# Optimization experiments

Measured on AMD Instinct MI355X. Metric: run time of the kernel, lower is better.

## Reference

```python
import jax, jax.numpy as jnp
import numpy as np

N_NODES = 100000
N_EDGES = 1600000
IN_CH = 128
OUT_CH = 64


def setup_inputs() -> dict:
    key = jax.random.key(0)
    k1, k2, k3, k4, k5 = jax.random.split(key, 5)
    x = jax.random.normal(k1, (N_NODES, IN_CH), dtype=jnp.float32)
    edge_index = jax.random.randint(k2, (2, N_EDGES), 0, N_NODES, dtype=jnp.int64)
    edge_weight = jax.random.uniform(k3, (N_EDGES,), dtype=jnp.float32)
    # GCNConv linear weight (glorot-ish scale) and bias
    W = jax.random.normal(k4, (IN_CH, OUT_CH), dtype=jnp.float32) / np.float32(np.sqrt(IN_CH))
    b = jax.random.normal(k5, (OUT_CH,), dtype=jnp.float32) * 0.01
    return {"x": x, "edge_index": edge_index, "edge_weight": edge_weight, "W": W, "b": b}


def reference(x, edge_index, edge_weight, W, b):
    # PyG GCNConv with add_self_loops=False, normalize=True, followed by Sigmoid.
    row = edge_index[0]  # source nodes [E]
    col = edge_index[1]  # target nodes [E]
    n = x.shape[0]

    # gcn_norm (no self loops): deg[j] = sum of edge_weight into j
    deg = jax.ops.segment_sum(edge_weight, col, num_segments=n)  # [N]
    deg_inv_sqrt = jnp.where(deg > 0, jax.lax.rsqrt(deg), jnp.float32(0))
    norm = deg_inv_sqrt[row] * edge_weight * deg_inv_sqrt[col]  # [E]

    # linear transform then gather-scale-scatter aggregation
    h = x @ W  # [N, OUT]
    msg = norm[:, None] * h[row]  # [E, OUT]
    out = jax.ops.segment_sum(msg, col, num_segments=n) + b  # [N, OUT]
    return jax.nn.sigmoid(out)
```

## Files before the change

### kernel.cpp

```cpp
#include <hip/hip_runtime.h>

#define IN_CH 128
#define OUT_CH 64
#define BN 64
#define CAP 1280
#define NPART 256

typedef __attribute__((ext_vector_type(8))) short short8;
typedef __attribute__((ext_vector_type(4))) float f32x4;

__device__ __forceinline__ unsigned short f2bf(float f) {
    unsigned u = __float_as_uint(f);
    unsigned r = (u + 0x7FFFu + ((u >> 16) & 1u)) >> 16;
    return (unsigned short)r;
}

__global__ __launch_bounds__(1024) void k_part1(const int* __restrict__ row,
                                                const int* __restrict__ col,
                                                const float* __restrict__ ew,
                                                int* __restrict__ cnt,
                                                uint2* __restrict__ sparse,
                                                int E, int per, int nbuck) {
    __shared__ int lh[1600];
    __shared__ int cur[1600];
    int tid = threadIdx.x;
    for (int i = tid; i < nbuck; i += 1024) lh[i] = 0;
    __syncthreads();
    int e0 = blockIdx.x * per;
    int e1 = min(E, e0 + per);
    for (int e = e0 + tid; e < e1; e += 1024)
        atomicAdd(&lh[col[e] >> 6], 1);
    __syncthreads();
    for (int bin = tid; bin < nbuck; bin += 1024) {
        int c = lh[bin];
        int base = c ? atomicAdd(&cnt[bin], c) : 0;
        cur[bin] = bin * CAP + base;
    }
    __syncthreads();
    int lim = nbuck * CAP;
    for (int e = e0 + tid; e < e1; e += 1024) {
        int r = row[e];
        int c = col[e];
        float w = ew[e];
        int bin = c >> 6;
        int p = atomicAdd(&cur[bin], 1);
        if (p < lim)
            sparse[p] = make_uint2((unsigned)r | ((unsigned)(c & 63) << 17),
                                   __float_as_uint(w));
    }
}

__global__ __launch_bounds__(256) void k_gemm3(const float* __restrict__ x,
                                               const float* __restrict__ W,
                                               const uint2* __restrict__ sparse,
                                               const int* __restrict__ cnt,
                                               float* __restrict__ dis,
                                               unsigned short* __restrict__ hb,
                                               int N) {
    __shared__ unsigned short Wl[64][136];
    __shared__ float degs[BN];

    int tid = threadIdx.x;
    int b = blockIdx.x;
    int row0 = b * BN;

    if (tid < BN) degs[tid] = 0.f;
    __syncthreads();

    for (int i = tid; i < 2048; i += 256) {
        int k = i >> 4;
        int n4 = (i & 15) << 2;
        float4 v = *(const float4*)(W + (size_t)k * OUT_CH + n4);
        Wl[n4 + 0][k] = f2bf(v.x);
        Wl[n4 + 1][k] = f2bf(v.y);
        Wl[n4 + 2][k] = f2bf(v.z);
        Wl[n4 + 3][k] = f2bf(v.w);
    }
    {
        int m = min(cnt[b], CAP);
        int sbase = b * CAP;
        for (int i = tid; i < m; i += 256) {
            uint2 r = sparse[sbase + i];
            atomicAdd(&degs[(r.x >> 17) & 63], __uint_as_float(r.y));
        }
    }
    __syncthreads();

    if (tid < BN) {
        float d = degs[tid];
        float dv = (d > 0.f) ? rsqrtf(d) : 0.f;
        int node = row0 + tid;
        if (node < N) dis[node] = dv;
        degs[tid] = dv;
    }

    int lane = tid & 63;
    int wv = tid >> 6;
    int r0l = 16 * wv;
    int cn = lane & 15;
    int rg = lane >> 4;

    f32x4 acc0 = {0.f, 0.f, 0.f, 0.f};
    f32x4 acc1 = {0.f, 0.f, 0.f, 0.f};
    f32x4 acc2 = {0.f, 0.f, 0.f, 0.f};
    f32x4 acc3 = {0.f, 0.f, 0.f, 0.f};

    int arow = row0 + r0l + cn;
#pragma unroll
    for (int ks = 0; ks < 4; ++ks) {
        int k0 = ks * 32 + rg * 8;
        short8 a = {};
        if (arow < N) {
            const float* xp = x + (size_t)arow * IN_CH + k0;
            float4 va = *(const float4*)(xp);
            float4 vb = *(const float4*)(xp + 4);
            a[0] = (short)f2bf(va.x); a[1] = (short)f2bf(va.y);
            a[2] = (short)f2bf(va.z); a[3] = (short)f2bf(va.w);
            a[4] = (short)f2bf(vb.x); a[5] = (short)f2bf(vb.y);
            a[6] = (short)f2bf(vb.z); a[7] = (short)f2bf(vb.w);
        }
        short8 b0 = *(const short8*)&Wl[ 0 + cn][k0];
        short8 b1 = *(const short8*)&Wl[16 + cn][k0];
        short8 b2 = *(const short8*)&Wl[32 + cn][k0];
        short8 b3 = *(const short8*)&Wl[48 + cn][k0];
        acc0 = __builtin_amdgcn_mfma_f32_16x16x32_bf16(a, b0, acc0, 0, 0, 0);
        acc1 = __builtin_amdgcn_mfma_f32_16x16x32_bf16(a, b1, acc1, 0, 0, 0);
        acc2 = __builtin_amdgcn_mfma_f32_16x16x32_bf16(a, b2, acc2, 0, 0, 0);
        acc3 = __builtin_amdgcn_mfma_f32_16x16x32_bf16(a, b3, acc3, 0, 0, 0);
    }
    __syncthreads();

#pragma unroll
    for (int r = 0; r < 4; ++r) {
        int row_l = r0l + rg * 4 + r;
        int grow = row0 + row_l;
        if (grow < N) {
            float sc = degs[row_l];
            unsigned short* hp = hb + (size_t)grow * OUT_CH + cn;
            hp[ 0] = f2bf(acc0[r] * sc);
            hp[16] = f2bf(acc1[r] * sc);
            hp[32] = f2bf(acc2[r] * sc);
            hp[48] = f2bf(acc3[r] * sc);
        }
    }
}

__global__ __launch_bounds__(256) void k_sort3(const uint2* __restrict__ sparse,
                                               const int* __restrict__ cnt,
                                               const float* __restrict__ dis,
                                               const unsigned short* __restrict__ hb,
                                               const float* __restrict__ bias,
                                               float* __restrict__ out,
                                               int N, int nbuck) {
    __shared__ uint2 recbuf[CAP];
    __shared__ uint2 recbuf2[CAP];
    __shared__ int hist[BN];
    __shared__ int cur[BN];
    __shared__ int starts[BN];

    int b = blockIdx.x;
    int tid = threadIdx.x;
    int sbase = b * CAP;
    int m = min(cnt[b], CAP);

    if (tid < BN) hist[tid] = 0;
    __syncthreads();

    for (int i = tid; i < m; i += 256) {
        uint2 r = sparse[sbase + i];
        recbuf[i] = r;
        atomicAdd(&hist[(r.x >> 17) & 63], 1);
    }
    __syncthreads();

    if (tid < 64) {
        int h = hist[tid];
        int v = h;
#pragma unroll
        for (int d = 1; d < 64; d <<= 1) {
            int t = __shfl_up(v, d, 64);
            if (tid >= d) v += t;
        }
        int excl = v - h;
        cur[tid] = excl;
        starts[tid] = excl;
    }
    __syncthreads();

    for (int i = tid; i < m; i += 256) {
        uint2 r = recbuf[i];
        int dl = (r.x >> 17) & 63;
        int p = atomicAdd(&cur[dl], 1);
        recbuf2[p] = make_uint2(r.x & 0x1FFFF, r.y);
    }
    __syncthreads();

    int hwl = tid >> 5;
    int lanep = tid & 31;
    unsigned co = 2u * (unsigned)lanep;
    for (int nl = hwl; nl < BN; nl += 8) {
        int node = b * BN + nl;
        if (node >= N) break;
        int e = starts[nl];
        int e1 = e + hist[nl];
        float accx = 0.f, accy = 0.f;
        for (; e + 3 < e1; e += 4) {
            uint2 p0 = recbuf2[e];
            uint2 p1 = recbuf2[e + 1];
            uint2 p2 = recbuf2[e + 2];
            uint2 p3 = recbuf2[e + 3];
            unsigned v0 = *(const unsigned*)(hb + (p0.x << 6) + co);
            unsigned v1 = *(const unsigned*)(hb + (p1.x << 6) + co);
            unsigned v2 = *(const unsigned*)(hb + (p2.x << 6) + co);
            unsigned v3 = *(const unsigned*)(hb + (p3.x << 6) + co);
            float w0 = __uint_as_float(p0.y), w1 = __uint_as_float(p1.y);
            float w2 = __uint_as_float(p2.y), w3 = __uint_as_float(p3.y);
            accx += w0 * __uint_as_float(v0 << 16);
            accy += w0 * __uint_as_float(v0 & 0xFFFF0000u);
            accx += w1 * __uint_as_float(v1 << 16);
            accy += w1 * __uint_as_float(v1 & 0xFFFF0000u);
            accx += w2 * __uint_as_float(v2 << 16);
            accy += w2 * __uint_as_float(v2 & 0xFFFF0000u);
            accx += w3 * __uint_as_float(v3 << 16);
            accy += w3 * __uint_as_float(v3 & 0xFFFF0000u);
        }
        for (; e < e1; ++e) {
            uint2 p = recbuf2[e];
            unsigned v = *(const unsigned*)(hb + (p.x << 6) + co);
            float w = __uint_as_float(p.y);
            accx += w * __uint_as_float(v << 16);
            accy += w * __uint_as_float(v & 0xFFFF0000u);
        }
        float dd = dis[node];
        float2 bb = *(const float2*)(bias + co);
        float2 o;
        o.x = 1.f / (1.f + __expf(-(accx * dd + bb.x)));
        o.y = 1.f / (1.f + __expf(-(accy * dd + bb.y)));
        *(float2*)(out + ((size_t)node << 6) + co) = o;
    }
}

extern "C" void kernel_launch(void* const* d_in, const int* in_sizes, int n_in,
                              void* d_out, int out_size, void* d_ws, size_t ws_size,
                              hipStream_t stream) {
    const float* x   = (const float*)d_in[0];
    const int*   ei  = (const int*)d_in[1];
    const float* ew  = (const float*)d_in[2];
    const float* W   = (const float*)d_in[3];
    const float* b   = (const float*)d_in[4];
    float* out = (float*)d_out;

    const int N = in_sizes[0] / IN_CH;
    const int E = in_sizes[1] / 2;
    const int* row = ei;
    const int* col = ei + E;

    const int nbuck = (N + BN - 1) / BN;
    const int per   = (E + NPART - 1) / NPART;

    char* p = (char*)d_ws;
    int*   cnt     = (int*)p;    p += (size_t)nbuck * 4;
    float* dis     = (float*)p;  p += (size_t)N * 4;
    uint2* sparse  = (uint2*)p;  p += (size_t)nbuck * CAP * 8;
    unsigned short* hb = (unsigned short*)p;

    hipMemsetAsync(cnt, 0, (size_t)nbuck * 4, stream);

    k_part1<<<NPART, 1024, 0, stream>>>(row, col, ew, cnt, sparse, E, per, nbuck);
    k_gemm3<<<nbuck, 256, 0, stream>>>(x, W, sparse, cnt, dis, hb, N);
    k_sort3<<<nbuck, 256, 0, stream>>>(sparse, cnt, dis, hb, b, out, N, nbuck);
}
```

Before: 199.7 us.

## Replace per-bucket counting sort with LDS float atomics in aggregation

The aggregation kernel no longer counting-sorts each bucket's edges by destination node. Instead, half-waves walk the edge records in arbitrary order and accumulate weighted bf16 features into a 64x64 float tile in shared memory with atomicAdd. A separate epilogue then applies degree scaling, bias and sigmoid with float4 stores. This removes the histogram, scan and scatter passes, at the cost of many LDS float atomics that may contend when several edges hit the same node. It also makes the summation order nondeterministic.

```diff
diff --git a/kernel.cpp b/kernel.cpp
--- a/kernel.cpp
+++ b/kernel.cpp
@@ -145,98 +145,76 @@
     }
 }
 
-__global__ __launch_bounds__(256) void k_sort3(const uint2* __restrict__ sparse,
-                                               const int* __restrict__ cnt,
-                                               const float* __restrict__ dis,
-                                               const unsigned short* __restrict__ hb,
-                                               const float* __restrict__ bias,
-                                               float* __restrict__ out,
-                                               int N, int nbuck) {
+__global__ __launch_bounds__(256) void k_agg(const uint2* __restrict__ sparse,
+                                             const int* __restrict__ cnt,
+                                             const float* __restrict__ dis,
+                                             const unsigned short* __restrict__ hb,
+                                             const float* __restrict__ bias,
+                                             float* __restrict__ out,
+                                             int N, int nbuck) {
     __shared__ uint2 recbuf[CAP];
-    __shared__ uint2 recbuf2[CAP];
-    __shared__ int hist[BN];
-    __shared__ int cur[BN];
-    __shared__ int starts[BN];
+    __shared__ float acc[BN][OUT_CH];
 
     int b = blockIdx.x;
     int tid = threadIdx.x;
     int sbase = b * CAP;
     int m = min(cnt[b], CAP);
-
-    if (tid < BN) hist[tid] = 0;
-    __syncthreads();
-
-    for (int i = tid; i < m; i += 256) {
-        uint2 r = sparse[sbase + i];
-        recbuf[i] = r;
-        atomicAdd(&hist[(r.x >> 17) & 63], 1);
-    }
-    __syncthreads();
-
-    if (tid < 64) {
-        int h = hist[tid];
-        int v = h;
-#pragma unroll
-        for (int d = 1; d < 64; d <<= 1) {
-            int t = __shfl_up(v, d, 64);
-            if (tid >= d) v += t;
-        }
-        int excl = v - h;
-        cur[tid] = excl;
-        starts[tid] = excl;
-    }
-    __syncthreads();
-
-    for (int i = tid; i < m; i += 256) {
-        uint2 r = recbuf[i];
-        int dl = (r.x >> 17) & 63;
-        int p = atomicAdd(&cur[dl], 1);
-        recbuf2[p] = make_uint2(r.x & 0x1FFFF, r.y);
-    }
-    __syncthreads();
-
-    int hwl = tid >> 5;
+    int mp = (m + 31) & ~31;
+
+    float* az = &acc[0][0];
+    for (int i = tid; i < BN * OUT_CH; i += 256) az[i] = 0.f;
+    for (int i = tid; i < mp; i += 256)
+        recbuf[i] = (i < m) ? sparse[sbase + i] : make_uint2(0u, 0u);
+    __syncthreads();
+
+    int hw = tid >> 5;
     int lanep = tid & 31;
     unsigned co = 2u * (unsigned)lanep;
-    for (int nl = hwl; nl < BN; nl += 8) {
-        int node = b * BN + nl;
-        if (node >= N) break;
-        int e = starts[nl];
-        int e1 = e + hist[nl];
-        float accx = 0.f, accy = 0.f;
-        for (; e + 3 < e1; e += 4) {
-            uint2 p0 = recbuf2[e];
-            uint2 p1 = recbuf2[e + 1];
-            uint2 p2 = recbuf2[e + 2];
-            uint2 p3 = recbuf2[e + 3];
-            unsigned v0 = *(const unsigned*)(hb + (p0.x << 6) + co);
-            unsigned v1 = *(const unsigned*)(hb + (p1.x << 6) + co);
-            unsigned v2 = *(const unsigned*)(hb + (p2.x << 6) + co);
-            unsigned v3 = *(const unsigned*)(hb + (p3.x << 6) + co);
-            float w0 = __uint_as_float(p0.y), w1 = __uint_as_float(p1.y);
-            float w2 = __uint_as_float(p2.y), w3 = __uint_as_float(p3.y);
-            accx += w0 * __uint_as_float(v0 << 16);
-            accy += w0 * __uint_as_float(v0 & 0xFFFF0000u);
-            accx += w1 * __uint_as_float(v1 << 16);
-            accy += w1 * __uint_as_float(v1 & 0xFFFF0000u);
-            accx += w2 * __uint_as_float(v2 << 16);
-            accy += w2 * __uint_as_float(v2 & 0xFFFF0000u);
-            accx += w3 * __uint_as_float(v3 << 16);
-            accy += w3 * __uint_as_float(v3 & 0xFFFF0000u);
-        }
-        for (; e < e1; ++e) {
-            uint2 p = recbuf2[e];
-            unsigned v = *(const unsigned*)(hb + (p.x << 6) + co);
-            float w = __uint_as_float(p.y);
-            accx += w * __uint_as_float(v << 16);
-            accy += w * __uint_as_float(v & 0xFFFF0000u);
-        }
+
+    for (int i = hw * 4; i < mp; i += 32) {
+        uint2 r0 = recbuf[i + 0];
+        uint2 r1 = recbuf[i + 1];
+        uint2 r2 = recbuf[i + 2];
+        uint2 r3 = recbuf[i + 3];
+        unsigned v0 = *(const unsigned*)(hb + (((size_t)(r0.x & 0x1FFFFu)) << 6) + co);
+        unsigned v1 = *(const unsigned*)(hb + (((size_t)(r1.x & 0x1FFFFu)) << 6) + co);
+        unsigned v2 = *(const unsigned*)(hb + (((size_t)(r2.x & 0x1FFFFu)) << 6) + co);
+        unsigned v3 = *(const unsigned*)(hb + (((size_t)(r3.x & 0x1FFFFu)) << 6) + co);
+        float w0 = __uint_as_float(r0.y);
+        float w1 = __uint_as_float(r1.y);
+        float w2 = __uint_as_float(r2.y);
+        float w3 = __uint_as_float(r3.y);
+        int d0 = (r0.x >> 17) & 63;
+        int d1 = (r1.x >> 17) & 63;
+        int d2 = (r2.x >> 17) & 63;
+        int d3 = (r3.x >> 17) & 63;
+        atomicAdd(&acc[d0][co],     w0 * __uint_as_float(v0 << 16));
+        atomicAdd(&acc[d0][co + 1], w0 * __uint_as_float(v0 & 0xFFFF0000u));
+        atomicAdd(&acc[d1][co],     w1 * __uint_as_float(v1 << 16));
+        atomicAdd(&acc[d1][co + 1], w1 * __uint_as_float(v1 & 0xFFFF0000u));
+        atomicAdd(&acc[d2][co],     w2 * __uint_as_float(v2 << 16));
+        atomicAdd(&acc[d2][co + 1], w2 * __uint_as_float(v2 & 0xFFFF0000u));
+        atomicAdd(&acc[d3][co],     w3 * __uint_as_float(v3 << 16));
+        atomicAdd(&acc[d3][co + 1], w3 * __uint_as_float(v3 & 0xFFFF0000u));
+    }
+    __syncthreads();
+
+    int nl = tid >> 2;
+    int node = b * BN + nl;
+    if (node < N) {
         float dd = dis[node];
-        float2 bb = *(const float2*)(bias + co);
-        float2 o;
-        o.x = 1.f / (1.f + __expf(-(accx * dd + bb.x)));
-        o.y = 1.f / (1.f + __expf(-(accy * dd + bb.y)));
-        *(float2*)(out + ((size_t)node << 6) + co) = o;
+        int c0 = (tid & 3) * 16;
+#pragma unroll
+        for (int j = 0; j < 4; ++j) {
+            float4 a = *(const float4*)&acc[nl][c0 + 4 * j];
+            float4 bb = *(const float4*)(bias + c0 + 4 * j);
+            float4 o;
+            o.x = 1.f / (1.f + __expf(-(a.x * dd + bb.x)));
+            o.y = 1.f / (1.f + __expf(-(a.y * dd + bb.y)));
+            o.z = 1.f / (1.f + __expf(-(a.z * dd + bb.z)));
+            o.w = 1.f / (1.f + __expf(-(a.w * dd + bb.w)));
+            *(float4*)(out + ((size_t)node << 6) + c0 + 4 * j) = o;
+        }
     }
 }
 
@@ -268,5 +246,5 @@
 
     k_part1<<<NPART, 1024, 0, stream>>>(row, col, ew, cnt, sparse, E, per, nbuck);
     k_gemm3<<<nbuck, 256, 0, stream>>>(x, W, sparse, cnt, dis, hb, N);
-    k_sort3<<<nbuck, 256, 0, stream>>>(sparse, cnt, dis, hb, b, out, N, nbuck);
-}
+    k_agg<<<nbuck, 256, 0, stream>>>(sparse, cnt, dis, hb, b, out, N, nbuck);
+}
```

After: 767.3 us. +284.2%, slower.

## Pad per-node edge lists and interleave two nodes per half-wave gather loop

Applied to the files above, without the earlier changes.

The sort/aggregate kernel drops the first shared staging buffer and re-reads records from global memory for the scatter pass, which halves LDS use so more blocks can be resident. Each node's edge segment is padded to a multiple of 4 with zero-weight dummies, so the scalar tail loop goes away. Each half-wave then processes two nodes (nl and nl+32) in one loop, issuing eight independent gathers per iteration for more memory-level parallelism. In exchange, the sparse records are read from global twice, and uneven degrees waste work on masked iterations.

```diff
diff --git a/kernel.cpp b/kernel.cpp
--- a/kernel.cpp
+++ b/kernel.cpp
@@ -145,18 +145,18 @@
     }
 }
 
-__global__ __launch_bounds__(256) void k_sort3(const uint2* __restrict__ sparse,
+__global__ __launch_bounds__(256) void k_sort4(const uint2* __restrict__ sparse,
                                                const int* __restrict__ cnt,
                                                const float* __restrict__ dis,
                                                const unsigned short* __restrict__ hb,
                                                const float* __restrict__ bias,
                                                float* __restrict__ out,
                                                int N, int nbuck) {
-    __shared__ uint2 recbuf[CAP];
-    __shared__ uint2 recbuf2[CAP];
+    __shared__ uint2 recbuf2[CAP + 256];
     __shared__ int hist[BN];
+    __shared__ int iters[BN];
+    __shared__ int starts[BN];
     __shared__ int cur[BN];
-    __shared__ int starts[BN];
 
     int b = blockIdx.x;
     int tid = threadIdx.x;
@@ -166,29 +166,38 @@
     if (tid < BN) hist[tid] = 0;
     __syncthreads();
 
-    for (int i = tid; i < m; i += 256) {
-        uint2 r = sparse[sbase + i];
-        recbuf[i] = r;
-        atomicAdd(&hist[(r.x >> 17) & 63], 1);
-    }
+    for (int i = tid; i < m; i += 256)
+        atomicAdd(&hist[(sparse[sbase + i].x >> 17) & 63], 1);
     __syncthreads();
 
     if (tid < 64) {
         int h = hist[tid];
-        int v = h;
+        int hp = (h + 3) & ~3;
+        int v = hp;
 #pragma unroll
         for (int d = 1; d < 64; d <<= 1) {
             int t = __shfl_up(v, d, 64);
             if (tid >= d) v += t;
         }
-        int excl = v - h;
-        cur[tid] = excl;
-        starts[tid] = excl;
-    }
-    __syncthreads();
-
+        starts[tid] = v - hp;
+        cur[tid] = v - hp;
+        iters[tid] = hp >> 2;
+        if (tid == 63) {
+            recbuf2[v + 0] = make_uint2(0u, 0u);
+            recbuf2[v + 1] = make_uint2(0u, 0u);
+            recbuf2[v + 2] = make_uint2(0u, 0u);
+            recbuf2[v + 3] = make_uint2(0u, 0u);
+        }
+    }
+    __syncthreads();
+
+    if (tid < BN) {
+        int s = starts[tid] + hist[tid];
+        int e = starts[tid] + (iters[tid] << 2);
+        for (int k = s; k < e; ++k) recbuf2[k] = make_uint2(0u, 0u);
+    }
     for (int i = tid; i < m; i += 256) {
-        uint2 r = recbuf[i];
+        uint2 r = sparse[sbase + i];
         int dl = (r.x >> 17) & 63;
         int p = atomicAdd(&cur[dl], 1);
         recbuf2[p] = make_uint2(r.x & 0x1FFFF, r.y);
@@ -198,45 +207,76 @@
     int hwl = tid >> 5;
     int lanep = tid & 31;
     unsigned co = 2u * (unsigned)lanep;
-    for (int nl = hwl; nl < BN; nl += 8) {
-        int node = b * BN + nl;
-        if (node >= N) break;
-        int e = starts[nl];
-        int e1 = e + hist[nl];
-        float accx = 0.f, accy = 0.f;
-        for (; e + 3 < e1; e += 4) {
-            uint2 p0 = recbuf2[e];
-            uint2 p1 = recbuf2[e + 1];
-            uint2 p2 = recbuf2[e + 2];
-            uint2 p3 = recbuf2[e + 3];
-            unsigned v0 = *(const unsigned*)(hb + (p0.x << 6) + co);
-            unsigned v1 = *(const unsigned*)(hb + (p1.x << 6) + co);
-            unsigned v2 = *(const unsigned*)(hb + (p2.x << 6) + co);
-            unsigned v3 = *(const unsigned*)(hb + (p3.x << 6) + co);
-            float w0 = __uint_as_float(p0.y), w1 = __uint_as_float(p1.y);
-            float w2 = __uint_as_float(p2.y), w3 = __uint_as_float(p3.y);
-            accx += w0 * __uint_as_float(v0 << 16);
-            accy += w0 * __uint_as_float(v0 & 0xFFFF0000u);
-            accx += w1 * __uint_as_float(v1 << 16);
-            accy += w1 * __uint_as_float(v1 & 0xFFFF0000u);
-            accx += w2 * __uint_as_float(v2 << 16);
-            accy += w2 * __uint_as_float(v2 & 0xFFFF0000u);
-            accx += w3 * __uint_as_float(v3 << 16);
-            accy += w3 * __uint_as_float(v3 & 0xFFFF0000u);
-        }
-        for (; e < e1; ++e) {
-            uint2 p = recbuf2[e];
-            unsigned v = *(const unsigned*)(hb + (p.x << 6) + co);
-            float w = __uint_as_float(p.y);
-            accx += w * __uint_as_float(v << 16);
-            accy += w * __uint_as_float(v & 0xFFFF0000u);
-        }
-        float dd = dis[node];
+
+    for (int np = hwl; np < 32; np += 8) {
+        int nA = np, nB = np + 32;
+        int eA = starts[nA], cA = iters[nA];
+        int eB = starts[nB], cB = iters[nB];
+        int it = max(cA, cB);
+        float axA = 0.f, ayA = 0.f, axB = 0.f, ayB = 0.f;
+
+        for (int k = 0; k < it; ++k) {
+            int kA = min(k, cA - 1); if (kA < 0) kA = 0;
+            int kB = min(k, cB - 1); if (kB < 0) kB = 0;
+            bool mA = k < cA;
+            bool mB = k < cB;
+            int ea = eA + 4 * kA;
+            int eb = eB + 4 * kB;
+            uint2 a0 = recbuf2[ea + 0], a1 = recbuf2[ea + 1];
+            uint2 a2 = recbuf2[ea + 2], a3 = recbuf2[ea + 3];
+            uint2 b0 = recbuf2[eb + 0], b1 = recbuf2[eb + 1];
+            uint2 b2 = recbuf2[eb + 2], b3 = recbuf2[eb + 3];
+            unsigned va0 = *(const unsigned*)(hb + (((size_t)a0.x) << 6) + co);
+            unsigned va1 = *(const unsigned*)(hb + (((size_t)a1.x) << 6) + co);
+            unsigned va2 = *(const unsigned*)(hb + (((size_t)a2.x) << 6) + co);
+            unsigned va3 = *(const unsigned*)(hb + (((size_t)a3.x) << 6) + co);
+            unsigned vb0 = *(const unsigned*)(hb + (((size_t)b0.x) << 6) + co);
+            unsigned vb1 = *(const unsigned*)(hb + (((size_t)b1.x) << 6) + co);
+            unsigned vb2 = *(const unsigned*)(hb + (((size_t)b2.x) << 6) + co);
+            unsigned vb3 = *(const unsigned*)(hb + (((size_t)b3.x) << 6) + co);
+            float wa0 = mA ? __uint_as_float(a0.y) : 0.f;
+            float wa1 = mA ? __uint_as_float(a1.y) : 0.f;
+            float wa2 = mA ? __uint_as_float(a2.y) : 0.f;
+            float wa3 = mA ? __uint_as_float(a3.y) : 0.f;
+            float wb0 = mB ? __uint_as_float(b0.y) : 0.f;
+            float wb1 = mB ? __uint_as_float(b1.y) : 0.f;
+            float wb2 = mB ? __uint_as_float(b2.y) : 0.f;
+            float wb3 = mB ? __uint_as_float(b3.y) : 0.f;
+            axA += wa0 * __uint_as_float(va0 << 16);
+            ayA += wa0 * __uint_as_float(va0 & 0xFFFF0000u);
+            axA += wa1 * __uint_as_float(va1 << 16);
+            ayA += wa1 * __uint_as_float(va1 & 0xFFFF0000u);
+            axA += wa2 * __uint_as_float(va2 << 16);
+            ayA += wa2 * __uint_as_float(va2 & 0xFFFF0000u);
+            axA += wa3 * __uint_as_float(va3 << 16);
+            ayA += wa3 * __uint_as_float(va3 & 0xFFFF0000u);
+            axB += wb0 * __uint_as_float(vb0 << 16);
+            ayB += wb0 * __uint_as_float(vb0 & 0xFFFF0000u);
+            axB += wb1 * __uint_as_float(vb1 << 16);
+            ayB += wb1 * __uint_as_float(vb1 & 0xFFFF0000u);
+            axB += wb2 * __uint_as_float(vb2 << 16);
+            ayB += wb2 * __uint_as_float(vb2 & 0xFFFF0000u);
+            axB += wb3 * __uint_as_float(vb3 << 16);
+            ayB += wb3 * __uint_as_float(vb3 & 0xFFFF0000u);
+        }
+
         float2 bb = *(const float2*)(bias + co);
-        float2 o;
-        o.x = 1.f / (1.f + __expf(-(accx * dd + bb.x)));
-        o.y = 1.f / (1.f + __expf(-(accy * dd + bb.y)));
-        *(float2*)(out + ((size_t)node << 6) + co) = o;
+        int nodeA = b * BN + nA;
+        int nodeB = b * BN + nB;
+        if (nodeA < N) {
+            float dd = dis[nodeA];
+            float2 o;
+            o.x = 1.f / (1.f + __expf(-(axA * dd + bb.x)));
+            o.y = 1.f / (1.f + __expf(-(ayA * dd + bb.y)));
+            *(float2*)(out + ((size_t)nodeA << 6) + co) = o;
+        }
+        if (nodeB < N) {
+            float dd = dis[nodeB];
+            float2 o;
+            o.x = 1.f / (1.f + __expf(-(axB * dd + bb.x)));
+            o.y = 1.f / (1.f + __expf(-(ayB * dd + bb.y)));
+            *(float2*)(out + ((size_t)nodeB << 6) + co) = o;
+        }
     }
 }
 
@@ -268,5 +308,5 @@
 
     k_part1<<<NPART, 1024, 0, stream>>>(row, col, ew, cnt, sparse, E, per, nbuck);
     k_gemm3<<<nbuck, 256, 0, stream>>>(x, W, sparse, cnt, dis, hb, N);
-    k_sort3<<<nbuck, 256, 0, stream>>>(sparse, cnt, dis, hb, b, out, N, nbuck);
-}
+    k_sort4<<<nbuck, 256, 0, stream>>>(sparse, cnt, dis, hb, b, out, N, nbuck);
+}
```

Measured after the change: 210.4 us. +5.4%, slower.

## Stage partitioned edges in LDS before writing buckets contiguously to global

Applied to the files above, without the earlier changes.

The partition kernel now does a block-wide prefix scan over per-bucket counts, stages the packed edge records in shared memory sorted by bucket, and then writes them out with consecutive threads writing consecutive positions within each bucket run. This replaces scattered 8-byte global stores with mostly contiguous ones, reducing uncoalesced write traffic. In exchange it uses about 80KB of LDS per block, which limits occupancy, and adds extra syncs and a scan. It also assumes each block's edge slice fits in the 6272-entry staging buffer.

```diff
diff --git a/kernel.cpp b/kernel.cpp
--- a/kernel.cpp
+++ b/kernel.cpp
@@ -15,38 +15,82 @@
     return (unsigned short)r;
 }
 
-__global__ __launch_bounds__(1024) void k_part1(const int* __restrict__ row,
+__global__ __launch_bounds__(1024) void k_part2(const int* __restrict__ row,
                                                 const int* __restrict__ col,
                                                 const float* __restrict__ ew,
                                                 int* __restrict__ cnt,
                                                 uint2* __restrict__ sparse,
                                                 int E, int per, int nbuck) {
-    __shared__ int lh[1600];
-    __shared__ int cur[1600];
+    __shared__ uint2 srec[6272];
+    __shared__ unsigned short sbin[6272];
+    __shared__ int loff[1600];
+    __shared__ int lcur[1600];
+    __shared__ int gbase[1600];
+    __shared__ int wpart[16];
+    __shared__ int stot;
+
     int tid = threadIdx.x;
-    for (int i = tid; i < nbuck; i += 1024) lh[i] = 0;
-    __syncthreads();
     int e0 = blockIdx.x * per;
     int e1 = min(E, e0 + per);
+    int nloc = e1 - e0;
+
+    for (int i = tid; i < nbuck; i += 1024) loff[i] = 0;
+    __syncthreads();
+
     for (int e = e0 + tid; e < e1; e += 1024)
-        atomicAdd(&lh[col[e] >> 6], 1);
-    __syncthreads();
-    for (int bin = tid; bin < nbuck; bin += 1024) {
-        int c = lh[bin];
-        int base = c ? atomicAdd(&cnt[bin], c) : 0;
-        cur[bin] = bin * CAP + base;
-    }
-    __syncthreads();
-    int lim = nbuck * CAP;
+        atomicAdd(&loff[col[e] >> 6], 1);
+    __syncthreads();
+
+    int b0 = 2 * tid, b1 = 2 * tid + 1;
+    int s0 = (b0 < nbuck) ? loff[b0] : 0;
+    int s1 = (b1 < nbuck) ? loff[b1] : 0;
+    int ts = s0 + s1;
+    int lane = tid & 63, wv = tid >> 6;
+    int v = ts;
+#pragma unroll
+    for (int d = 1; d < 64; d <<= 1) { int t = __shfl_up(v, d, 64); if (lane >= d) v += t; }
+    if (lane == 63) wpart[wv] = v;
+    __syncthreads();
+    if (tid < 16) {
+        int vv = wpart[tid];
+#pragma unroll
+        for (int d = 1; d < 16; d <<= 1) { int t = __shfl_up(vv, d, 16); if (tid >= d) vv += t; }
+        wpart[tid] = vv;
+        if (tid == 15) stot = vv;
+    }
+    __syncthreads();
+    int excl = ((wv > 0) ? wpart[wv - 1] : 0) + (v - ts);
+    if (b0 < nbuck) loff[b0] = excl;
+    if (b1 < nbuck) loff[b1] = excl + s0;
+    __syncthreads();
+
+    int total = stot;
+    for (int b = tid; b < nbuck; b += 1024) {
+        int nxt = (b + 1 < nbuck) ? loff[b + 1] : total;
+        int c = nxt - loff[b];
+        gbase[b] = c ? atomicAdd(&cnt[b], c) : 0;
+        lcur[b] = loff[b];
+    }
+    __syncthreads();
+
     for (int e = e0 + tid; e < e1; e += 1024) {
         int r = row[e];
         int c = col[e];
         float w = ew[e];
         int bin = c >> 6;
-        int p = atomicAdd(&cur[bin], 1);
-        if (p < lim)
-            sparse[p] = make_uint2((unsigned)r | ((unsigned)(c & 63) << 17),
-                                   __float_as_uint(w));
+        int p = atomicAdd(&lcur[bin], 1);
+        srec[p] = make_uint2((unsigned)r | ((unsigned)(c & 63) << 17),
+                             __float_as_uint(w));
+        sbin[p] = (unsigned short)bin;
+    }
+    __syncthreads();
+
+    for (int i = tid; i < nloc; i += 1024) {
+        int bin = sbin[i];
+        int k = i - loff[bin];
+        int gp = gbase[bin] + k;
+        if (gp < CAP)
+            sparse[(size_t)bin * CAP + gp] = srec[i];
     }
 }
 
@@ -266,7 +310,7 @@
 
     hipMemsetAsync(cnt, 0, (size_t)nbuck * 4, stream);
 
-    k_part1<<<NPART, 1024, 0, stream>>>(row, col, ew, cnt, sparse, E, per, nbuck);
+    k_part2<<<NPART, 1024, 0, stream>>>(row, col, ew, cnt, sparse, E, per, nbuck);
     k_gemm3<<<nbuck, 256, 0, stream>>>(x, W, sparse, cnt, dis, hb, N);
     k_sort3<<<nbuck, 256, 0, stream>>>(sparse, cnt, dis, hb, b, out, N, nbuck);
 }
```

New measurement: 192.1 us. 1.04x faster.
